# Kernel tuning notes

Hardware: AMD Instinct MI355X
Metric: run time of the kernel (lower is better)

## Reference

```python
import jax, jax.numpy as jnp
import numpy as np

N_EMBED = 384
BLOCK_SIZE = 256
HEAD_SIZE = 64
B, T = 256, 256


def setup_inputs() -> dict:
    key = jax.random.key(0)
    k1, k2, k3, k4 = jax.random.split(key, 4)
    x = jax.random.normal(k1, (B, T, N_EMBED), dtype=jnp.float32)
    Wq = jax.random.normal(k2, (N_EMBED, HEAD_SIZE), dtype=jnp.float32) * (N_EMBED ** -0.5)
    Wk = jax.random.normal(k3, (N_EMBED, HEAD_SIZE), dtype=jnp.float32) * (N_EMBED ** -0.5)
    Wv = jax.random.normal(k4, (N_EMBED, HEAD_SIZE), dtype=jnp.float32) * (N_EMBED ** -0.5)
    return {"x": x, "Wq": Wq, "Wk": Wk, "Wv": Wv}


def reference(x, Wq, Wk, Wv):
    Bb, Tt, C = x.shape
    q = jnp.einsum("btc,ch->bth", x, Wq)
    k = jnp.einsum("btc,ch->bth", x, Wk)
    v = jnp.einsum("btc,ch->bth", x, Wv)
    # NOTE: original scales by C**-0.5 where C = n_embed (384), not head_size
    scale = jnp.asarray(C, x.dtype) ** -0.5
    wei = jnp.einsum("bqh,bkh->bqk", q, k) * scale  # [B, T, T]
    causal = jnp.tril(jnp.ones((Tt, Tt), dtype=bool))
    wei = jnp.where(causal, wei, -jnp.inf)
    wei = jax.nn.softmax(wei, axis=-1)
    out = jnp.einsum("bqk,bkh->bqh", wei, v)
    return out
```

## Files before the change

kernel.cpp:

```cpp
#include <hip/hip_runtime.h>
#include <hip/hip_bf16.h>
#include <math.h>

#define BB   256
#define TT   256
#define CIN  384
#define HS   64
#define BT   (BB*TT)

#define QSCL ((float)(0.051031036307982884 * 1.4426950408889634))

typedef __attribute__((ext_vector_type(8))) short short8;
typedef __attribute__((ext_vector_type(4))) float floatx4;

__device__ inline short bf16bits(float f) {
    union { __hip_bfloat16 h; short s; } u;
    u.h = __float2bfloat16(f);
    return u.s;
}

__device__ inline short8 cvt8(const float4& f0, const float4& f1) {
    union { __hip_bfloat162 h[4]; short8 s8; } u;
    u.h[0] = __float22bfloat162_rn(make_float2(f0.x, f0.y));
    u.h[1] = __float22bfloat162_rn(make_float2(f0.z, f0.w));
    u.h[2] = __float22bfloat162_rn(make_float2(f1.x, f1.y));
    u.h[3] = __float22bfloat162_rn(make_float2(f1.z, f1.w));
    return u.s8;
}

__global__ __launch_bounds__(256) void prep_wtp(
    const float* __restrict__ Wq, const float* __restrict__ Wk,
    const float* __restrict__ Wv, short* __restrict__ WtP)
{
    const int idx  = blockIdx.x * 256 + threadIdx.x;
    const int j    = idx & 7;
    const int quad = (idx >> 3) & 3;
    const int l15  = (idx >> 5) & 15;
    int X          = idx >> 9;
    const int nt   = X % 6;  X /= 6;
    const int ks   = X & 1;  X >>= 1;
    const int s    = X % 6;  X /= 6;
    const int wn   = X;

    const int n  = wn * 96 + nt * 16 + l15;
    const int kk = s * 64 + ks * 32 + quad * 8 + j;
    const float* W = (n < 64) ? Wq : (n < 128) ? Wk : Wv;
    WtP[idx] = bf16bits(W[kk * 64 + (n & 63)]);
}

__global__ __launch_bounds__(512, 2) void fused_head(
    const float* __restrict__ x, const short* __restrict__ WtP,
    float* __restrict__ out)
{
    __shared__ short smem[58880];

    const int tid  = threadIdx.x;
    const int b    = blockIdx.x;
    const int lane = tid & 63;
    const int w    = tid >> 6;
    const int l15  = lane & 15;
    const int quad = lane >> 4;
    const int kq   = quad * 8;
    const int crow = quad * 4;

    const float* xb = x + (size_t)b * 256 * 384;
    const int laneoff = l15 * 32 + quad * 8;

    floatx4 acc[2][12] = {};

    const float* xr0 = xb + (size_t)(w * 32 +      l15) * 384 + kq;
    const float* xr1 = xb + (size_t)(w * 32 + 16 + l15) * 384 + kq;

    float4 A[3][2][2][2];
#pragma unroll
    for (int p = 0; p < 3; ++p) {
#pragma unroll
        for (int ks = 0; ks < 2; ++ks) {
            A[p][0][ks][0] = *(const float4*)(xr0 + p * 64 + ks * 32);
            A[p][0][ks][1] = *(const float4*)(xr0 + p * 64 + ks * 32 + 4);
            A[p][1][ks][0] = *(const float4*)(xr1 + p * 64 + ks * 32);
            A[p][1][ks][1] = *(const float4*)(xr1 + p * 64 + ks * 32 + 4);
        }
    }

#pragma unroll
    for (int s = 0; s < 6; ++s) {
        const int bi = s % 3;

#pragma unroll
        for (int ks = 0; ks < 2; ++ks) {
            const short8 af0 = cvt8(A[bi][0][ks][0], A[bi][0][ks][1]);
            const short8 af1 = cvt8(A[bi][1][ks][0], A[bi][1][ks][1]);
            short8 bf[12];
#pragma unroll
            for (int h = 0; h < 2; ++h)
#pragma unroll
                for (int nt = 0; nt < 6; ++nt)
                    bf[h * 6 + nt] = *(const short8*)
                        &WtP[((((h * 6 + s) * 2 + ks) * 6 + nt) << 9) + laneoff];
#pragma unroll
            for (int j = 0; j < 12; ++j) {
                acc[0][j] = __builtin_amdgcn_mfma_f32_16x16x32_bf16(
                    af0, bf[j], acc[0][j], 0, 0, 0);
                acc[1][j] = __builtin_amdgcn_mfma_f32_16x16x32_bf16(
                    af1, bf[j], acc[1][j], 0, 0, 0);
            }
        }

        if (s < 3) {
#pragma unroll
            for (int ks = 0; ks < 2; ++ks) {
                A[bi][0][ks][0] = *(const float4*)(xr0 + (s + 3) * 64 + ks * 32);
                A[bi][0][ks][1] = *(const float4*)(xr0 + (s + 3) * 64 + ks * 32 + 4);
                A[bi][1][ks][0] = *(const float4*)(xr1 + (s + 3) * 64 + ks * 32);
                A[bi][1][ks][1] = *(const float4*)(xr1 + (s + 3) * 64 + ks * 32 + 4);
            }
        }
    }

    short* q_lds = smem;
    short* k_lds = smem + 18432;
    short* vt    = smem + 36864;
    short* Ps    = smem + 53760;

#pragma unroll
    for (int mt = 0; mt < 2; ++mt)
#pragma unroll
        for (int j = 0; j < 12; ++j) {
            const int n = j * 16 + l15;
#pragma unroll
            for (int r = 0; r < 4; ++r) {
                const int m = w * 32 + mt * 16 + crow + r;
                const float av = acc[mt][j][r];
                if (j < 4)      q_lds[m * 72 + n]          = bf16bits(av * QSCL);
                else if (j < 8) k_lds[m * 72 + (n - 64)]   = bf16bits(av);
                else            vt[(n - 128) * 264 + m]    = bf16bits(av);
            }
        }
    __syncthreads();

#pragma unroll
    for (int g = 0; g < 2; ++g) {
        const int grp = g ? (15 - w) : w;
        const int r0  = grp * 16;

        short8 aq0, aq1;
        aq0 = *(const short8*)&q_lds[(r0 + l15) * 72 + kq];
        aq1 = *(const short8*)&q_lds[(r0 + l15) * 72 + 32 + kq];

        float lsum[4] = {0.f, 0.f, 0.f, 0.f};
        floatx4 O[4] = {};

        const int nch = (r0 + 47) >> 5;
        for (int c = 0; c < nch; ++c) {
            const int cb = c * 32;

            floatx4 st[2];
#pragma unroll
            for (int t = 0; t < 2; ++t) {
                const short8 b0 = *(const short8*)&k_lds[(cb + t * 16 + l15) * 72 + kq];
                const short8 b1 = *(const short8*)&k_lds[(cb + t * 16 + l15) * 72 + 32 + kq];
                floatx4 z = {};
                z = __builtin_amdgcn_mfma_f32_16x16x32_bf16(aq0, b0, z, 0, 0, 0);
                z = __builtin_amdgcn_mfma_f32_16x16x32_bf16(aq1, b1, z, 0, 0, 0);
                st[t] = z;
            }

#pragma unroll
            for (int t = 0; t < 2; ++t)
#pragma unroll
                for (int r = 0; r < 4; ++r) {
                    const int key  = cb + t * 16 + l15;
                    const int qrow = r0 + crow + r;
                    float p = __builtin_amdgcn_exp2f(st[t][r]);
                    p = (key <= qrow) ? p : 0.f;
                    lsum[r] += p;
                    Ps[w * 640 + (crow + r) * 40 + t * 16 + l15] = bf16bits(p);
                }

            asm volatile("s_waitcnt lgkmcnt(0)" ::: "memory");

            const short8 pa = *(const short8*)&Ps[w * 640 + l15 * 40 + kq];
#pragma unroll
            for (int n = 0; n < 4; ++n) {
                const short8 bv = *(const short8*)&vt[(n * 16 + l15) * 264 + cb + kq];
                O[n] = __builtin_amdgcn_mfma_f32_16x16x32_bf16(pa, bv, O[n], 0, 0, 0);
            }
        }

#pragma unroll
        for (int off = 1; off < 16; off <<= 1)
#pragma unroll
            for (int r = 0; r < 4; ++r)
                lsum[r] += __shfl_xor(lsum[r], off, 16);

        float inv[4];
#pragma unroll
        for (int r = 0; r < 4; ++r) inv[r] = 1.f / lsum[r];
#pragma unroll
        for (int n = 0; n < 4; ++n)
#pragma unroll
            for (int r = 0; r < 4; ++r)
                out[(size_t)(b * 256 + r0 + crow + r) * 64 + n * 16 + l15] = O[n][r] * inv[r];
    }
}

extern "C" void kernel_launch(void* const* d_in, const int* in_sizes, int n_in,
                              void* d_out, int out_size, void* d_ws, size_t ws_size,
                              hipStream_t stream)
{
    const float* x  = (const float*)d_in[0];
    const float* Wq = (const float*)d_in[1];
    const float* Wk = (const float*)d_in[2];
    const float* Wv = (const float*)d_in[3];
    float* out = (float*)d_out;

    short* WtP = (short*)d_ws;

    prep_wtp<<<(192 * 384) / 256, 256, 0, stream>>>(Wq, Wk, Wv, WtP);
    fused_head<<<BB, 512, 0, stream>>>(x, WtP, out);
}
```

Before: 185.0 us.

## Double waves per block, halve rows per wave, repack Q/K/V LDS fragments

The fused head kernel now launches 1024 threads (16 waves) per batch block instead of 512. Each wave projects 16 rows instead of 32 and prefetches x one stage ahead instead of keeping a three-deep register buffer. Q, K and V are stored in LDS as unpadded 16x32 MFMA fragment tiles, so the attention loads use contiguous packed addresses. Each wave now handles one 16-row query group instead of two balanced (w, 15-w) groups. The aim is more waves per CU to hide latency, paid for by twice the weight-fragment loads per row and a causal imbalance across waves, with possible LDS bank conflicts from the unpadded layout.

```diff
diff --git a/kernel.cpp b/kernel.cpp
--- a/kernel.cpp
+++ b/kernel.cpp
@@ -6,7 +6,6 @@
 #define TT   256
 #define CIN  384
 #define HS   64
-#define BT   (BB*TT)
 
 #define QSCL ((float)(0.051031036307982884 * 1.4426950408889634))
 
@@ -48,11 +47,11 @@
     WtP[idx] = bf16bits(W[kk * 64 + (n & 63)]);
 }
 
-__global__ __launch_bounds__(512, 2) void fused_head(
+__global__ __launch_bounds__(1024, 4) void fused_head(
     const float* __restrict__ x, const short* __restrict__ WtP,
     float* __restrict__ out)
 {
-    __shared__ short smem[58880];
+    __shared__ short smem[59392];
 
     const int tid  = threadIdx.x;
     const int b    = blockIdx.x;
@@ -64,89 +63,82 @@
     const int crow = quad * 4;
 
     const float* xb = x + (size_t)b * 256 * 384;
-    const int laneoff = l15 * 32 + quad * 8;
-
-    floatx4 acc[2][12] = {};
-
-    const float* xr0 = xb + (size_t)(w * 32 +      l15) * 384 + kq;
-    const float* xr1 = xb + (size_t)(w * 32 + 16 + l15) * 384 + kq;
-
-    float4 A[3][2][2][2];
-#pragma unroll
-    for (int p = 0; p < 3; ++p) {
+    const int laneoff = l15 * 32 + kq;
+
+    floatx4 acc[12] = {};
+
+    const float* xr = xb + (size_t)(w * 16 + l15) * 384 + kq;
+
+    float4 c00 = *(const float4*)(xr + 0);
+    float4 c01 = *(const float4*)(xr + 4);
+    float4 c10 = *(const float4*)(xr + 32);
+    float4 c11 = *(const float4*)(xr + 36);
+
+#pragma unroll
+    for (int s = 0; s < 6; ++s) {
+        float4 n00, n01, n10, n11;
+        if (s < 5) {
+            n00 = *(const float4*)(xr + (s + 1) * 64 + 0);
+            n01 = *(const float4*)(xr + (s + 1) * 64 + 4);
+            n10 = *(const float4*)(xr + (s + 1) * 64 + 32);
+            n11 = *(const float4*)(xr + (s + 1) * 64 + 36);
+        }
+        const short8 af0 = cvt8(c00, c01);
+        const short8 af1 = cvt8(c10, c11);
 #pragma unroll
         for (int ks = 0; ks < 2; ++ks) {
-            A[p][0][ks][0] = *(const float4*)(xr0 + p * 64 + ks * 32);
-            A[p][0][ks][1] = *(const float4*)(xr0 + p * 64 + ks * 32 + 4);
-            A[p][1][ks][0] = *(const float4*)(xr1 + p * 64 + ks * 32);
-            A[p][1][ks][1] = *(const float4*)(xr1 + p * 64 + ks * 32 + 4);
-        }
+            const short8 af = ks ? af1 : af0;
+#pragma unroll
+            for (int h = 0; h < 2; ++h) {
+                short8 bf[6];
+#pragma unroll
+                for (int nt = 0; nt < 6; ++nt)
+                    bf[nt] = *(const short8*)
+                        &WtP[((((h * 6 + s) * 2 + ks) * 6 + nt) << 9) + laneoff];
+#pragma unroll
+                for (int nt = 0; nt < 6; ++nt)
+                    acc[h * 6 + nt] = __builtin_amdgcn_mfma_f32_16x16x32_bf16(
+                        af, bf[nt], acc[h * 6 + nt], 0, 0, 0);
+            }
+        }
+        if (s < 5) { c00 = n00; c01 = n01; c10 = n10; c11 = n11; }
     }
 
-#pragma unroll
-    for (int s = 0; s < 6; ++s) {
-        const int bi = s % 3;
-
-#pragma unroll
-        for (int ks = 0; ks < 2; ++ks) {
-            const short8 af0 = cvt8(A[bi][0][ks][0], A[bi][0][ks][1]);
-            const short8 af1 = cvt8(A[bi][1][ks][0], A[bi][1][ks][1]);
-            short8 bf[12];
-#pragma unroll
-            for (int h = 0; h < 2; ++h)
-#pragma unroll
-                for (int nt = 0; nt < 6; ++nt)
-                    bf[h * 6 + nt] = *(const short8*)
-                        &WtP[((((h * 6 + s) * 2 + ks) * 6 + nt) << 9) + laneoff];
-#pragma unroll
-            for (int j = 0; j < 12; ++j) {
-                acc[0][j] = __builtin_amdgcn_mfma_f32_16x16x32_bf16(
-                    af0, bf[j], acc[0][j], 0, 0, 0);
-                acc[1][j] = __builtin_amdgcn_mfma_f32_16x16x32_bf16(
-                    af1, bf[j], acc[1][j], 0, 0, 0);
-            }
-        }
-
-        if (s < 3) {
-#pragma unroll
-            for (int ks = 0; ks < 2; ++ks) {
-                A[bi][0][ks][0] = *(const float4*)(xr0 + (s + 3) * 64 + ks * 32);
-                A[bi][0][ks][1] = *(const float4*)(xr0 + (s + 3) * 64 + ks * 32 + 4);
-                A[bi][1][ks][0] = *(const float4*)(xr1 + (s + 3) * 64 + ks * 32);
-                A[bi][1][ks][1] = *(const float4*)(xr1 + (s + 3) * 64 + ks * 32 + 4);
+    short* qP = smem;
+    short* kP = smem + 16384;
+    short* vP = smem + 32768;
+    short* Ps = smem + 49152;
+
+#pragma unroll
+    for (int j = 0; j < 12; ++j) {
+#pragma unroll
+        for (int r = 0; r < 4; ++r) {
+            const int n  = j * 16 + l15;
+            const int mr = crow + r;
+            const float av = acc[j][r];
+            if (j < 4) {
+                const int h = j >> 1;
+                qP[((w * 2 + h) * 16 + mr) * 32 + ((n & 31) >> 3) * 8 + (n & 7)]
+                    = bf16bits(av * QSCL);
+            } else if (j < 8) {
+                const int h = (j - 4) >> 1;
+                kP[((w * 2 + h) * 16 + mr) * 32 + (((n - 64) & 31) >> 3) * 8 + (n & 7)]
+                    = bf16bits(av);
+            } else {
+                const int nb = j - 8;
+                const int kk = (w & 1) * 16 + mr;
+                vP[(((w >> 1) * 4 + nb) * 16 + l15) * 32 + kk] = bf16bits(av);
             }
         }
     }
-
-    short* q_lds = smem;
-    short* k_lds = smem + 18432;
-    short* vt    = smem + 36864;
-    short* Ps    = smem + 53760;
-
-#pragma unroll
-    for (int mt = 0; mt < 2; ++mt)
-#pragma unroll
-        for (int j = 0; j < 12; ++j) {
-            const int n = j * 16 + l15;
-#pragma unroll
-            for (int r = 0; r < 4; ++r) {
-                const int m = w * 32 + mt * 16 + crow + r;
-                const float av = acc[mt][j][r];
-                if (j < 4)      q_lds[m * 72 + n]          = bf16bits(av * QSCL);
-                else if (j < 8) k_lds[m * 72 + (n - 64)]   = bf16bits(av);
-                else            vt[(n - 128) * 264 + m]    = bf16bits(av);
-            }
-        }
     __syncthreads();
 
-#pragma unroll
-    for (int g = 0; g < 2; ++g) {
-        const int grp = g ? (15 - w) : w;
-        const int r0  = grp * 16;
-
-        short8 aq0, aq1;
-        aq0 = *(const short8*)&q_lds[(r0 + l15) * 72 + kq];
-        aq1 = *(const short8*)&q_lds[(r0 + l15) * 72 + 32 + kq];
+    {
+        const int g  = w;
+        const int r0 = g * 16;
+
+        const short8 aq0 = *(const short8*)&qP[((g * 2 + 0) * 16 + l15) * 32 + kq];
+        const short8 aq1 = *(const short8*)&qP[((g * 2 + 1) * 16 + l15) * 32 + kq];
 
         float lsum[4] = {0.f, 0.f, 0.f, 0.f};
         floatx4 O[4] = {};
@@ -158,8 +150,10 @@
             floatx4 st[2];
 #pragma unroll
             for (int t = 0; t < 2; ++t) {
-                const short8 b0 = *(const short8*)&k_lds[(cb + t * 16 + l15) * 72 + kq];
-                const short8 b1 = *(const short8*)&k_lds[(cb + t * 16 + l15) * 72 + 32 + kq];
+                const short8 b0 = *(const short8*)
+                    &kP[(((c * 2 + t) * 2 + 0) * 16 + l15) * 32 + kq];
+                const short8 b1 = *(const short8*)
+                    &kP[(((c * 2 + t) * 2 + 1) * 16 + l15) * 32 + kq];
                 floatx4 z = {};
                 z = __builtin_amdgcn_mfma_f32_16x16x32_bf16(aq0, b0, z, 0, 0, 0);
                 z = __builtin_amdgcn_mfma_f32_16x16x32_bf16(aq1, b1, z, 0, 0, 0);
@@ -183,7 +177,8 @@
             const short8 pa = *(const short8*)&Ps[w * 640 + l15 * 40 + kq];
 #pragma unroll
             for (int n = 0; n < 4; ++n) {
-                const short8 bv = *(const short8*)&vt[(n * 16 + l15) * 264 + cb + kq];
+                const short8 bv = *(const short8*)
+                    &vP[((c * 4 + n) * 16 + l15) * 32 + kq];
                 O[n] = __builtin_amdgcn_mfma_f32_16x16x32_bf16(pa, bv, O[n], 0, 0, 0);
             }
         }
@@ -201,7 +196,8 @@
         for (int n = 0; n < 4; ++n)
 #pragma unroll
             for (int r = 0; r < 4; ++r)
-                out[(size_t)(b * 256 + r0 + crow + r) * 64 + n * 16 + l15] = O[n][r] * inv[r];
+                out[(size_t)(b * 256 + r0 + crow + r) * 64 + n * 16 + l15]
+                    = O[n][r] * inv[r];
     }
 }
 
@@ -218,5 +214,5 @@
     short* WtP = (short*)d_ws;
 
     prep_wtp<<<(192 * 384) / 256, 256, 0, stream>>>(Wq, Wk, Wv, WtP);
-    fused_head<<<BB, 512, 0, stream>>>(x, WtP, out);
-}
+    fused_head<<<BB, 1024, 0, stream>>>(x, WtP, out);
+}
```

Measured after the change: 181.1 us. 1.02x faster.
